# Performance work log

Measured on AMD Instinct MI355X. Metric: run time of the kernel, lower is better.

The kernel has to match this reference:

```python
import jax, jax.numpy as jnp
import numpy as np

EMBED_DIM = 1024
NUM_HEADS = 16
HEAD_DIM = EMBED_DIM // NUM_HEADS
B, T = 8, 1024


def setup_inputs() -> dict:
    key = jax.random.key(0)
    ks = jax.random.split(key, 8)
    s = EMBED_DIM ** -0.5
    return {
        "query": jax.random.normal(ks[0], (B, T, EMBED_DIM), jnp.float32),
        "key": jax.random.normal(ks[1], (B, T, EMBED_DIM), jnp.float32),
        "value": jax.random.normal(ks[2], (B, T, EMBED_DIM), jnp.float32),
        "key_padding_mask": jnp.zeros((B, T), dtype=bool),
        "attn_mask": jax.random.normal(ks[3], (T, T), jnp.float32) * 0.02,
        "in_proj_weight": jax.random.normal(ks[4], (3 * EMBED_DIM, EMBED_DIM), jnp.float32) * s,
        "in_proj_bias": jax.random.normal(ks[5], (3 * EMBED_DIM,), jnp.float32) * 0.02,
        "out_proj_weight": jax.random.normal(ks[6], (EMBED_DIM, EMBED_DIM), jnp.float32) * s,
        "out_proj_bias": jax.random.normal(ks[7], (EMBED_DIM,), jnp.float32) * 0.02,
    }


def reference(query, key, value, key_padding_mask, attn_mask,
              in_proj_weight, in_proj_bias, out_proj_weight, out_proj_bias):
    E, H, Dh = EMBED_DIM, NUM_HEADS, HEAD_DIM
    scale = Dh ** -0.5
    w_q, w_k, w_v = in_proj_weight[:E], in_proj_weight[E:2 * E], in_proj_weight[2 * E:]
    b_q, b_k, b_v = in_proj_bias[:E], in_proj_bias[E:2 * E], in_proj_bias[2 * E:]

    b, t_q, _ = query.shape
    t_k = key.shape[1]
    # projections: F.linear(x, W, b) = x @ W.T + b
    q = (query @ w_q.T + b_q).reshape(b, t_q, H, Dh).transpose(0, 2, 1, 3)
    k = (key @ w_k.T + b_k).reshape(b, t_k, H, Dh).transpose(0, 2, 1, 3)
    v = (value @ w_v.T + b_v).reshape(b, t_k, H, Dh).transpose(0, 2, 1, 3)

    scores = jnp.einsum('bhqd,bhkd->bhqk', q, k) * scale  # [B,H,Tq,Tk]
    scores = jnp.where(key_padding_mask[:, None, None, :], -jnp.inf, scores)
    scores = scores + attn_mask  # broadcast [Tq,Tk] over batch/heads
    attn = jax.nn.softmax(scores, axis=-1)
    out = jnp.einsum('bhqk,bhkd->bhqd', attn, v)
    out = out.transpose(0, 2, 1, 3).reshape(b, t_q, E)
    return out @ out_proj_weight.T + out_proj_bias
```

## Files before the change

### kernel.cpp

```cpp
#include <hip/hip_runtime.h>
#include <cstdint>
#include <cstddef>

#define E_DIM   1024
#define NHEADS  16
#define DHEAD   64
#define BATCH   8
#define SEQ     1024
#define MROWS   (BATCH*SEQ)

#define LOG2E 1.44269504f

typedef __bf16 bf16;
typedef __attribute__((ext_vector_type(8))) __bf16 bf16x8;
typedef __attribute__((ext_vector_type(4))) __bf16 bf16x4;
typedef __attribute__((ext_vector_type(4))) float f32x4;

typedef const __attribute__((address_space(1))) unsigned int gu32;
typedef __attribute__((address_space(3))) unsigned int lu32;

__global__ __launch_bounds__(256)
void split_kernel(const float* __restrict__ src, bf16* __restrict__ hi,
                  bf16* __restrict__ lo, int n4)
{
    int i = blockIdx.x * 256 + threadIdx.x;
    if (i >= n4) return;
    float4 x = ((const float4*)src)[i];
    bf16x4 h, l;
    h[0] = (bf16)x.x; l[0] = (bf16)(x.x - (float)h[0]);
    h[1] = (bf16)x.y; l[1] = (bf16)(x.y - (float)h[1]);
    h[2] = (bf16)x.z; l[2] = (bf16)(x.z - (float)h[2]);
    h[3] = (bf16)x.w; l[3] = (bf16)(x.w - (float)h[3]);
    ((bf16x4*)hi)[i] = h;
    ((bf16x4*)lo)[i] = l;
}

__global__ __launch_bounds__(256)
void cvt_bf16_kernel(const float* __restrict__ src, bf16* __restrict__ dst,
                     float scale, int n4)
{
    int i = blockIdx.x * 256 + threadIdx.x;
    if (i >= n4) return;
    float4 x = ((const float4*)src)[i];
    bf16x4 h;
    h[0] = (bf16)(x.x * scale); h[1] = (bf16)(x.y * scale);
    h[2] = (bf16)(x.z * scale); h[3] = (bf16)(x.w * scale);
    ((bf16x4*)dst)[i] = h;
}

__global__ __launch_bounds__(512, 4)
void gemm_nt_mfma(const bf16* __restrict__ Ahi, const bf16* __restrict__ Alo,
                  const bf16* __restrict__ Whi, const bf16* __restrict__ Wlo,
                  const float* __restrict__ bias,
                  float* __restrict__ outF, bf16* __restrict__ outHi,
                  int M, int N, int K, int mode)
{
    __shared__ bf16 Ahs[2][128 * 32];
    __shared__ bf16 Als[2][128 * 32];
    __shared__ bf16 Whs[2][128 * 32];
    __shared__ bf16 Wls[2][128 * 32];

    const int tid  = threadIdx.x;
    const int lane = tid & 63;
    const int wid  = tid >> 6;
    const int wm = (wid >> 1) * 32;
    const int wn = (wid & 1) * 64;
    const int fr = lane & 15;
    const int fq = lane >> 4;
    const int fk = ((fq + (fr >> 1)) & 3) * 8;

    const int mBase = blockIdx.y * 128;
    const int nBase = blockIdx.x * 128;

    const int rowA0 = tid >> 2;
    const int colA0 = (((tid & 3) - ((tid >> 3) & 3)) & 3) * 8;

    const int dcol = lane & 15;
    float bv[4];
#pragma unroll
    for (int bn = 0; bn < 4; ++bn)
        bv[bn] = bias[nBase + wn + bn * 16 + dcol];

    f32x4 acc[2][4];
#pragma unroll
    for (int i = 0; i < 2; ++i)
#pragma unroll
        for (int j = 0; j < 4; ++j) acc[i][j] = (f32x4){0.f, 0.f, 0.f, 0.f};

    const bf16* pAh = Ahi + (size_t)(mBase + rowA0) * K + colA0;
    const bf16* pAl = Alo + (size_t)(mBase + rowA0) * K + colA0;
    const bf16* pWh = Whi + (size_t)(nBase + rowA0) * K + colA0;
    const bf16* pWl = Wlo + (size_t)(nBase + rowA0) * K + colA0;

    auto stage = [&](int bi) {
        __builtin_amdgcn_global_load_lds((gu32*)pAh, (lu32*)&Ahs[bi][wid * 512], 16, 0, 0);
        __builtin_amdgcn_global_load_lds((gu32*)pAl, (lu32*)&Als[bi][wid * 512], 16, 0, 0);
        __builtin_amdgcn_global_load_lds((gu32*)pWh, (lu32*)&Whs[bi][wid * 512], 16, 0, 0);
        __builtin_amdgcn_global_load_lds((gu32*)pWl, (lu32*)&Wls[bi][wid * 512], 16, 0, 0);
        pAh += 32; pAl += 32; pWh += 32; pWl += 32;
    };

    stage(0);

    const int NIT = K >> 5;
#pragma unroll 1
    for (int it = 0; it < NIT; ++it) {
        const int cur = it & 1;
        if (it + 1 < NIT) {
            stage(cur ^ 1);
            asm volatile("s_waitcnt vmcnt(4)" ::: "memory");
        } else {
            asm volatile("s_waitcnt vmcnt(0)" ::: "memory");
        }
        __builtin_amdgcn_s_barrier();

        const bf16* As = Ahs[cur];
        const bf16* Al = Als[cur];
        const bf16* Ws = Whs[cur];
        const bf16* Wl = Wls[cur];

        bf16x8 afh[2], afl[2], bfh[4], bfl[4];
#pragma unroll
        for (int am = 0; am < 2; ++am) {
            afh[am] = *(const bf16x8*)&As[(wm + am * 16 + fr) * 32 + fk];
            afl[am] = *(const bf16x8*)&Al[(wm + am * 16 + fr) * 32 + fk];
        }
#pragma unroll
        for (int bn = 0; bn < 4; ++bn) {
            bfh[bn] = *(const bf16x8*)&Ws[(wn + bn * 16 + fr) * 32 + fk];
            bfl[bn] = *(const bf16x8*)&Wl[(wn + bn * 16 + fr) * 32 + fk];
        }
        __builtin_amdgcn_s_setprio(1);
#pragma unroll
        for (int am = 0; am < 2; ++am)
#pragma unroll
            for (int bn = 0; bn < 4; ++bn) {
                acc[am][bn] = __builtin_amdgcn_mfma_f32_16x16x32_bf16(afh[am], bfh[bn], acc[am][bn], 0, 0, 0);
                acc[am][bn] = __builtin_amdgcn_mfma_f32_16x16x32_bf16(afh[am], bfl[bn], acc[am][bn], 0, 0, 0);
                acc[am][bn] = __builtin_amdgcn_mfma_f32_16x16x32_bf16(afl[am], bfh[bn], acc[am][bn], 0, 0, 0);
            }
        __builtin_amdgcn_s_setprio(0);
        __builtin_amdgcn_s_barrier();
    }

    const int drow = (lane >> 4) * 4;
#pragma unroll
    for (int bn = 0; bn < 4; ++bn) {
        const int col = nBase + wn + bn * 16 + dcol;
#pragma unroll
        for (int am = 0; am < 2; ++am) {
#pragma unroll
            for (int r = 0; r < 4; ++r) {
                const int row = mBase + wm + am * 16 + drow + r;
                const float v = acc[am][bn][r] + bv[bn];
                if (mode == 0) {
                    outF[(size_t)row * N + col] = v;
                } else {
                    const int b = row >> 10, t = row & 1023;
                    const int h = col >> 6,  d = col & 63;
                    size_t idx;
                    if (mode == 1)
                        idx = (((size_t)(b * NHEADS + h)) * SEQ + t) * DHEAD + d;
                    else
                        idx = (((size_t)(b * NHEADS + h)) * DHEAD + d) * SEQ + t;
                    outHi[idx] = (bf16)v;
                }
            }
        }
    }
}

__global__ __launch_bounds__(256)
void attn_mfma_kernel(const bf16* __restrict__ qkv,
                      const bf16* __restrict__ mask_bf,
                      const unsigned char* __restrict__ kpad,
                      bf16* __restrict__ ctx_hi, bf16* __restrict__ ctx_lo)
{
    __shared__ bf16 Ks [2][4096];
    __shared__ bf16 Vts[2][4096];
    __shared__ bf16 Pn[4][1024];

    const int tid  = threadIdx.x;
    const int lane = tid & 63;
    const int wid  = tid >> 6;
    const int c16  = lane & 15;
    const int quad = lane >> 4;

    const int bh = blockIdx.x;
    const int qt = blockIdx.y;
    const int b = bh >> 4, h = bh & 15;

    const size_t seg = (size_t)MROWS * E_DIM;
    const size_t headoff = (size_t)bh * SEQ * DHEAD;
    const bf16* Q_g  = qkv + headoff;
    const bf16* K_g  = qkv + seg + headoff;
    const bf16* Vt_g = qkv + 2 * seg + headoff;

    const int qglob = qt * 64 + wid * 16 + c16;

    bf16x8 qf[2];
#pragma unroll
    for (int ks = 0; ks < 2; ++ks)
        qf[ks] = *(const bf16x8*)&Q_g[(size_t)qglob * DHEAD + quad * 8 + ks * 32];

    float l_i = 0.f;
    f32x4 oacc[4];
#pragma unroll
    for (int dt = 0; dt < 4; ++dt) oacc[dt] = (f32x4){0.f, 0.f, 0.f, 0.f};

    const int row0 = tid >> 3,         c0 = (tid & 7) ^ (row0 & 7);
    const int row1 = (tid + 256) >> 3, c1 = ((tid + 256) & 7) ^ (row1 & 7);

    auto stage = [&](int kt, int bi) {
        const int ktb = kt * 64;
        const size_t k0 = (size_t)(ktb + row0) * DHEAD + c0 * 8;
        const size_t k1 = (size_t)(ktb + row1) * DHEAD + c1 * 8;
        const size_t v0 = (size_t)row0 * SEQ + ktb + c0 * 8;
        const size_t v1 = (size_t)row1 * SEQ + ktb + c1 * 8;
        __builtin_amdgcn_global_load_lds((gu32*)(K_g + k0),  (lu32*)&Ks [bi][wid * 512],        16, 0, 0);
        __builtin_amdgcn_global_load_lds((gu32*)(K_g + k1),  (lu32*)&Ks [bi][2048 + wid * 512], 16, 0, 0);
        __builtin_amdgcn_global_load_lds((gu32*)(Vt_g + v0), (lu32*)&Vts[bi][wid * 512],        16, 0, 0);
        __builtin_amdgcn_global_load_lds((gu32*)(Vt_g + v1), (lu32*)&Vts[bi][2048 + wid * 512], 16, 0, 0);
    };

    stage(0, 0);
    __syncthreads();

    const int pxor = (c16 & 7) << 3;
    const size_t kpb = (size_t)b * SEQ + quad * 4;

#pragma unroll 1
    for (int kt = 0; kt < 16; ++kt) {
        const int cur = kt & 1;
        const int ktb = kt * 64;

        bf16x4 mvh[4];
        unsigned kpu[4];
#pragma unroll
        for (int st = 0; st < 4; ++st) {
            mvh[st] = *(const bf16x4*)&mask_bf[(size_t)qglob * SEQ + ktb + st * 16 + quad * 4];
            kpu[st] = *(const unsigned*)&kpad[kpb + ktb + st * 16];
        }

        if (kt < 15) stage(kt + 1, cur ^ 1);

        f32x4 sacc[4];
#pragma unroll
        for (int st = 0; st < 4; ++st) sacc[st] = (f32x4){0.f, 0.f, 0.f, 0.f};
        __builtin_amdgcn_s_setprio(1);
#pragma unroll
        for (int st = 0; st < 4; ++st) {
            const int row = st * 16 + c16;
            const int sw  = row & 7;
#pragma unroll
            for (int ks = 0; ks < 2; ++ks) {
                const int cp = ((quad + ks * 4) ^ sw);
                bf16x8 kh = *(const bf16x8*)&Ks[cur][(row * 8 + cp) * 8];
                sacc[st] = __builtin_amdgcn_mfma_f32_16x16x32_bf16(kh, qf[ks], sacc[st], 0, 0, 0);
            }
        }
        __builtin_amdgcn_s_setprio(0);

        float s[16];
#pragma unroll
        for (int st = 0; st < 4; ++st) {
#pragma unroll
            for (int r = 0; r < 4; ++r)
                s[st * 4 + r] = fmaf(sacc[st][r], 0.125f * LOG2E, (float)mvh[st][r]);
        }
        if (__any((kpu[0] | kpu[1] | kpu[2] | kpu[3]) != 0u)) {
#pragma unroll
            for (int st = 0; st < 4; ++st)
#pragma unroll
                for (int r = 0; r < 4; ++r)
                    if ((kpu[st] >> (r * 8)) & 0xff) s[st * 4 + r] = -2e30f;
        }
        float p[16];
#pragma unroll
        for (int i = 0; i < 16; ++i)
            p[i] = __builtin_amdgcn_exp2f(fminf(s[i], 30.f));
        float u8[8];
#pragma unroll
        for (int i = 0; i < 8; ++i) u8[i] = p[i] + p[i + 8];
#pragma unroll
        for (int i = 0; i < 4; ++i) u8[i] += u8[i + 4];
        float ps = (u8[0] + u8[1]) + (u8[2] + u8[3]);
        ps += __shfl_xor(ps, 16, 64);
        ps += __shfl_xor(ps, 32, 64);
        l_i += ps;

#pragma unroll
        for (int st = 0; st < 4; ++st) {
            bf16x4 ph;
#pragma unroll
            for (int r = 0; r < 4; ++r) ph[r] = (bf16)p[st * 4 + r];
            *(bf16x4*)&Pn[wid][c16 * 64 + ((st * 16 + quad * 4) ^ pxor)] = ph;
        }
        bf16x8 pf[2];
#pragma unroll
        for (int ks = 0; ks < 2; ++ks)
            pf[ks] = *(const bf16x8*)&Pn[wid][c16 * 64 + ((ks * 32 + quad * 8) ^ pxor)];

        __builtin_amdgcn_s_setprio(1);
#pragma unroll
        for (int dt = 0; dt < 4; ++dt) {
            const int row = dt * 16 + c16;
            const int sw  = row & 7;
#pragma unroll
            for (int ks = 0; ks < 2; ++ks) {
                const int cp = ((quad + ks * 4) ^ sw);
                bf16x8 vh = *(const bf16x8*)&Vts[cur][(row * 8 + cp) * 8];
                oacc[dt] = __builtin_amdgcn_mfma_f32_16x16x32_bf16(vh, pf[ks], oacc[dt], 0, 0, 0);
            }
        }
        __builtin_amdgcn_s_setprio(0);

        __syncthreads();
    }

    const float invl = 1.0f / l_i;
#pragma unroll
    for (int dt = 0; dt < 4; ++dt) {
        bf16x4 oh, ol;
#pragma unroll
        for (int r = 0; r < 4; ++r) {
            float v = oacc[dt][r] * invl;
            oh[r] = (bf16)v;
            ol[r] = (bf16)(v - (float)oh[r]);
        }
        size_t idx = ((size_t)b * SEQ + qglob) * E_DIM + h * DHEAD + dt * 16 + quad * 4;
        *(bf16x4*)&ctx_hi[idx] = oh;
        *(bf16x4*)&ctx_lo[idx] = ol;
    }
}

extern "C" void kernel_launch(void* const* d_in, const int* in_sizes, int n_in,
                              void* d_out, int out_size, void* d_ws, size_t ws_size,
                              hipStream_t stream)
{
    const float* inputs[3] = { (const float*)d_in[0], (const float*)d_in[1],
                               (const float*)d_in[2] };
    const unsigned char* kpad = (const unsigned char*)d_in[3];
    const float* attn_mask = (const float*)d_in[4];
    const float* w_in  = (const float*)d_in[5];
    const float* b_in  = (const float*)d_in[6];
    const float* w_out = (const float*)d_in[7];
    const float* b_out = (const float*)d_in[8];
    float* out = (float*)d_out;

    char* ws = (char*)d_ws;
    const size_t MB = 1024 * 1024;
    bf16* bufA_hi  = (bf16*)(ws + 0 * MB);
    bf16* bufA_lo  = (bf16*)(ws + 16 * MB);
    bf16* w_in_hi  = (bf16*)(ws + 32 * MB);
    bf16* w_in_lo  = (bf16*)(ws + 38 * MB);
    bf16* w_out_hi = (bf16*)(ws + 44 * MB);
    bf16* w_out_lo = (bf16*)(ws + 46 * MB);
    bf16* qkv      = (bf16*)(ws + 48 * MB);
    bf16* mask_bf  = (bf16*)(ws + 96 * MB);
    bf16* ctx_hi   = (bf16*)(ws + 0 * MB);
    bf16* ctx_lo   = (bf16*)(ws + 16 * MB);

    const size_t seg = (size_t)MROWS * E_DIM;

    split_kernel<<<(3 * E_DIM * E_DIM / 4 + 255) / 256, 256, 0, stream>>>(
        w_in, w_in_hi, w_in_lo, 3 * E_DIM * E_DIM / 4);
    split_kernel<<<(E_DIM * E_DIM / 4 + 255) / 256, 256, 0, stream>>>(
        w_out, w_out_hi, w_out_lo, E_DIM * E_DIM / 4);
    cvt_bf16_kernel<<<(SEQ * SEQ / 4 + 255) / 256, 256, 0, stream>>>(
        attn_mask, mask_bf, LOG2E, SEQ * SEQ / 4);

    for (int z = 0; z < 3; ++z) {
        split_kernel<<<(int)(seg / 4 / 256), 256, 0, stream>>>(
            inputs[z], bufA_hi, bufA_lo, (int)(seg / 4));
        gemm_nt_mfma<<<dim3(E_DIM / 128, MROWS / 128), 512, 0, stream>>>(
            bufA_hi, bufA_lo,
            w_in_hi + (size_t)z * E_DIM * E_DIM, w_in_lo + (size_t)z * E_DIM * E_DIM,
            b_in + z * E_DIM,
            nullptr, qkv + (size_t)z * seg,
            MROWS, E_DIM, E_DIM, (z == 2) ? 2 : 1);
    }

    attn_mfma_kernel<<<dim3(BATCH * NHEADS, SEQ / 64), 256, 0, stream>>>(
        qkv, mask_bf, kpad, ctx_hi, ctx_lo);

    gemm_nt_mfma<<<dim3(E_DIM / 128, MROWS / 128), 512, 0, stream>>>(
        ctx_hi, ctx_lo, w_out_hi, w_out_lo, b_out,
        out, nullptr, MROWS, E_DIM, E_DIM, 0);
}
```

Measured before the change: 489.0 us.

## Fuse fp32 activation split into input-projection GEMM; widen attention blocks to 128 queries

The input projection GEMM now loads fp32 activations straight into LDS and does the hi/lo bf16 split in registers. This removes three separate split kernels and their intermediate global buffers. The attention kernel is widened to 512 threads covering 128 queries per block, so each staged K/V tile is shared by twice as many waves. The trade-off is more conversion work per GEMM k-step, a different LDS footprint and occupancy hint, and larger attention blocks.

```diff
diff --git a/kernel.cpp b/kernel.cpp
--- a/kernel.cpp
+++ b/kernel.cpp
@@ -48,17 +48,18 @@
     ((bf16x4*)dst)[i] = h;
 }
 
-__global__ __launch_bounds__(512, 4)
-void gemm_nt_mfma(const bf16* __restrict__ Ahi, const bf16* __restrict__ Alo,
+template<int AMODE>
+__global__ __launch_bounds__(512, 2)
+void gemm_nt_mfma(const float* __restrict__ Af,
+                  const bf16* __restrict__ Ahi, const bf16* __restrict__ Alo,
                   const bf16* __restrict__ Whi, const bf16* __restrict__ Wlo,
                   const float* __restrict__ bias,
                   float* __restrict__ outF, bf16* __restrict__ outHi,
                   int M, int N, int K, int mode)
 {
-    __shared__ bf16 Ahs[2][128 * 32];
-    __shared__ bf16 Als[2][128 * 32];
-    __shared__ bf16 Whs[2][128 * 32];
-    __shared__ bf16 Wls[2][128 * 32];
+    __shared__ char  smemA[2][16384];
+    __shared__ bf16  Whs[2][128 * 32];
+    __shared__ bf16  Wls[2][128 * 32];
 
     const int tid  = threadIdx.x;
     const int lane = tid & 63;
@@ -72,8 +73,10 @@
     const int mBase = blockIdx.y * 128;
     const int nBase = blockIdx.x * 128;
 
-    const int rowA0 = tid >> 2;
-    const int colA0 = (((tid & 3) - ((tid >> 3) & 3)) & 3) * 8;
+    const int rowW  = tid >> 2;
+    const int colW  = (((tid & 3) - ((tid >> 3) & 3)) & 3) * 8;
+    const int rowAf  = tid >> 3;
+    const int slotAf = ((tid & 7) - (rowAf & 7)) & 7;
 
     const int dcol = lane & 15;
     float bv[4];
@@ -87,17 +90,29 @@
 #pragma unroll
         for (int j = 0; j < 4; ++j) acc[i][j] = (f32x4){0.f, 0.f, 0.f, 0.f};
 
-    const bf16* pAh = Ahi + (size_t)(mBase + rowA0) * K + colA0;
-    const bf16* pAl = Alo + (size_t)(mBase + rowA0) * K + colA0;
-    const bf16* pWh = Whi + (size_t)(nBase + rowA0) * K + colA0;
-    const bf16* pWl = Wlo + (size_t)(nBase + rowA0) * K + colA0;
+    const float* pAf0 = Af  + (size_t)(mBase + rowAf) * K + slotAf * 4;
+    const float* pAf1 = pAf0 + (size_t)64 * K;
+    const bf16*  pAh  = Ahi + (size_t)(mBase + rowW) * K + colW;
+    const bf16*  pAl  = Alo + (size_t)(mBase + rowW) * K + colW;
+    const bf16*  pWh  = Whi + (size_t)(nBase + rowW) * K + colW;
+    const bf16*  pWl  = Wlo + (size_t)(nBase + rowW) * K + colW;
 
     auto stage = [&](int bi) {
-        __builtin_amdgcn_global_load_lds((gu32*)pAh, (lu32*)&Ahs[bi][wid * 512], 16, 0, 0);
-        __builtin_amdgcn_global_load_lds((gu32*)pAl, (lu32*)&Als[bi][wid * 512], 16, 0, 0);
+        if (AMODE == 1) {
+            float* As = (float*)smemA[bi];
+            __builtin_amdgcn_global_load_lds((gu32*)pAf0, (lu32*)&As[wid * 256],        16, 0, 0);
+            __builtin_amdgcn_global_load_lds((gu32*)pAf1, (lu32*)&As[2048 + wid * 256], 16, 0, 0);
+            pAf0 += 32; pAf1 += 32;
+        } else {
+            bf16* Ah = (bf16*)smemA[bi];
+            bf16* Al = Ah + 4096;
+            __builtin_amdgcn_global_load_lds((gu32*)pAh, (lu32*)&Ah[wid * 512], 16, 0, 0);
+            __builtin_amdgcn_global_load_lds((gu32*)pAl, (lu32*)&Al[wid * 512], 16, 0, 0);
+            pAh += 32; pAl += 32;
+        }
         __builtin_amdgcn_global_load_lds((gu32*)pWh, (lu32*)&Whs[bi][wid * 512], 16, 0, 0);
         __builtin_amdgcn_global_load_lds((gu32*)pWl, (lu32*)&Wls[bi][wid * 512], 16, 0, 0);
-        pAh += 32; pAl += 32; pWh += 32; pWl += 32;
+        pWh += 32; pWl += 32;
     };
 
     stage(0);
@@ -114,21 +129,38 @@
         }
         __builtin_amdgcn_s_barrier();
 
-        const bf16* As = Ahs[cur];
-        const bf16* Al = Als[cur];
-        const bf16* Ws = Whs[cur];
-        const bf16* Wl = Wls[cur];
-
         bf16x8 afh[2], afl[2], bfh[4], bfl[4];
-#pragma unroll
-        for (int am = 0; am < 2; ++am) {
-            afh[am] = *(const bf16x8*)&As[(wm + am * 16 + fr) * 32 + fk];
-            afl[am] = *(const bf16x8*)&Al[(wm + am * 16 + fr) * 32 + fk];
+        if (AMODE == 1) {
+            const float* As = (const float*)smemA[cur];
+#pragma unroll
+            for (int am = 0; am < 2; ++am) {
+                const int row = wm + am * 16 + fr;
+                const float* Ar = &As[row * 32];
+                f32x4 a0 = *(const f32x4*)&Ar[((2 * fq     + (fr & 7)) & 7) * 4];
+                f32x4 a1 = *(const f32x4*)&Ar[((2 * fq + 1 + (fr & 7)) & 7) * 4];
+                bf16x8 h, l;
+#pragma unroll
+                for (int j = 0; j < 4; ++j) {
+                    h[j]     = (bf16)a0[j];
+                    l[j]     = (bf16)(a0[j] - (float)h[j]);
+                    h[j + 4] = (bf16)a1[j];
+                    l[j + 4] = (bf16)(a1[j] - (float)h[j + 4]);
+                }
+                afh[am] = h; afl[am] = l;
+            }
+        } else {
+            const bf16* Ah = (const bf16*)smemA[cur];
+            const bf16* Al = Ah + 4096;
+#pragma unroll
+            for (int am = 0; am < 2; ++am) {
+                afh[am] = *(const bf16x8*)&Ah[(wm + am * 16 + fr) * 32 + fk];
+                afl[am] = *(const bf16x8*)&Al[(wm + am * 16 + fr) * 32 + fk];
+            }
         }
 #pragma unroll
         for (int bn = 0; bn < 4; ++bn) {
-            bfh[bn] = *(const bf16x8*)&Ws[(wn + bn * 16 + fr) * 32 + fk];
-            bfl[bn] = *(const bf16x8*)&Wl[(wn + bn * 16 + fr) * 32 + fk];
+            bfh[bn] = *(const bf16x8*)&Whs[cur][(wn + bn * 16 + fr) * 32 + fk];
+            bfl[bn] = *(const bf16x8*)&Wls[cur][(wn + bn * 16 + fr) * 32 + fk];
         }
         __builtin_amdgcn_s_setprio(1);
 #pragma unroll
@@ -170,7 +202,7 @@
     }
 }
 
-__global__ __launch_bounds__(256)
+__global__ __launch_bounds__(512)
 void attn_mfma_kernel(const bf16* __restrict__ qkv,
                       const bf16* __restrict__ mask_bf,
                       const unsigned char* __restrict__ kpad,
@@ -178,7 +210,7 @@
 {
     __shared__ bf16 Ks [2][4096];
     __shared__ bf16 Vts[2][4096];
-    __shared__ bf16 Pn[4][1024];
+    __shared__ bf16 Pn[8][1024];
 
     const int tid  = threadIdx.x;
     const int lane = tid & 63;
@@ -196,7 +228,7 @@
     const bf16* K_g  = qkv + seg + headoff;
     const bf16* Vt_g = qkv + 2 * seg + headoff;
 
-    const int qglob = qt * 64 + wid * 16 + c16;
+    const int qglob = qt * 128 + wid * 16 + c16;
 
     bf16x8 qf[2];
 #pragma unroll
@@ -208,19 +240,15 @@
 #pragma unroll
     for (int dt = 0; dt < 4; ++dt) oacc[dt] = (f32x4){0.f, 0.f, 0.f, 0.f};
 
-    const int row0 = tid >> 3,         c0 = (tid & 7) ^ (row0 & 7);
-    const int row1 = (tid + 256) >> 3, c1 = ((tid + 256) & 7) ^ (row1 & 7);
+    const int row0 = tid >> 3;
+    const int c0   = (tid & 7) ^ (row0 & 7);
 
     auto stage = [&](int kt, int bi) {
         const int ktb = kt * 64;
         const size_t k0 = (size_t)(ktb + row0) * DHEAD + c0 * 8;
-        const size_t k1 = (size_t)(ktb + row1) * DHEAD + c1 * 8;
         const size_t v0 = (size_t)row0 * SEQ + ktb + c0 * 8;
-        const size_t v1 = (size_t)row1 * SEQ + ktb + c1 * 8;
-        __builtin_amdgcn_global_load_lds((gu32*)(K_g + k0),  (lu32*)&Ks [bi][wid * 512],        16, 0, 0);
-        __builtin_amdgcn_global_load_lds((gu32*)(K_g + k1),  (lu32*)&Ks [bi][2048 + wid * 512], 16, 0, 0);
-        __builtin_amdgcn_global_load_lds((gu32*)(Vt_g + v0), (lu32*)&Vts[bi][wid * 512],        16, 0, 0);
-        __builtin_amdgcn_global_load_lds((gu32*)(Vt_g + v1), (lu32*)&Vts[bi][2048 + wid * 512], 16, 0, 0);
+        __builtin_amdgcn_global_load_lds((gu32*)(K_g + k0),  (lu32*)&Ks [bi][wid * 512], 16, 0, 0);
+        __builtin_amdgcn_global_load_lds((gu32*)(Vt_g + v0), (lu32*)&Vts[bi][wid * 512], 16, 0, 0);
     };
 
     stage(0, 0);
@@ -350,16 +378,14 @@
 
     char* ws = (char*)d_ws;
     const size_t MB = 1024 * 1024;
-    bf16* bufA_hi  = (bf16*)(ws + 0 * MB);
-    bf16* bufA_lo  = (bf16*)(ws + 16 * MB);
-    bf16* w_in_hi  = (bf16*)(ws + 32 * MB);
-    bf16* w_in_lo  = (bf16*)(ws + 38 * MB);
-    bf16* w_out_hi = (bf16*)(ws + 44 * MB);
-    bf16* w_out_lo = (bf16*)(ws + 46 * MB);
-    bf16* qkv      = (bf16*)(ws + 48 * MB);
-    bf16* mask_bf  = (bf16*)(ws + 96 * MB);
-    bf16* ctx_hi   = (bf16*)(ws + 0 * MB);
-    bf16* ctx_lo   = (bf16*)(ws + 16 * MB);
+    bf16* w_in_hi  = (bf16*)(ws + 0 * MB);
+    bf16* w_in_lo  = (bf16*)(ws + 6 * MB);
+    bf16* w_out_hi = (bf16*)(ws + 12 * MB);
+    bf16* w_out_lo = (bf16*)(ws + 14 * MB);
+    bf16* qkv      = (bf16*)(ws + 16 * MB);
+    bf16* mask_bf  = (bf16*)(ws + 64 * MB);
+    bf16* ctx_hi   = (bf16*)(ws + 66 * MB);
+    bf16* ctx_lo   = (bf16*)(ws + 82 * MB);
 
     const size_t seg = (size_t)MROWS * E_DIM;
 
@@ -371,20 +397,18 @@
         attn_mask, mask_bf, LOG2E, SEQ * SEQ / 4);
 
     for (int z = 0; z < 3; ++z) {
-        split_kernel<<<(int)(seg / 4 / 256), 256, 0, stream>>>(
-            inputs[z], bufA_hi, bufA_lo, (int)(seg / 4));
-        gemm_nt_mfma<<<dim3(E_DIM / 128, MROWS / 128), 512, 0, stream>>>(
-            bufA_hi, bufA_lo,
+        gemm_nt_mfma<1><<<dim3(E_DIM / 128, MROWS / 128), 512, 0, stream>>>(
+            inputs[z], nullptr, nullptr,
             w_in_hi + (size_t)z * E_DIM * E_DIM, w_in_lo + (size_t)z * E_DIM * E_DIM,
             b_in + z * E_DIM,
             nullptr, qkv + (size_t)z * seg,
             MROWS, E_DIM, E_DIM, (z == 2) ? 2 : 1);
     }
 
-    attn_mfma_kernel<<<dim3(BATCH * NHEADS, SEQ / 64), 256, 0, stream>>>(
+    attn_mfma_kernel<<<dim3(BATCH * NHEADS, SEQ / 128), 512, 0, stream>>>(
         qkv, mask_bf, kpad, ctx_hi, ctx_lo);
 
-    gemm_nt_mfma<<<dim3(E_DIM / 128, MROWS / 128), 512, 0, stream>>>(
-        ctx_hi, ctx_lo, w_out_hi, w_out_lo, b_out,
+    gemm_nt_mfma<0><<<dim3(E_DIM / 128, MROWS / 128), 512, 0, stream>>>(
+        nullptr, ctx_hi, ctx_lo, w_out_hi, w_out_lo, b_out,
         out, nullptr, MROWS, E_DIM, E_DIM, 0);
 }
```

New measurement: 466.0 us. 4.7% less time.
